# Kernel optimization log

Measured on AMD Instinct MI355X. Metric: run time of the kernel, lower is better.

## Reference

```python
import jax, jax.numpy as jnp
import numpy as np

KSZ, STRIDE, UNFOLD, FREQ = 9, 1, 12, 6  # patch size, stride, LISTA unfoldings, sim-refresh freq
P, C = 256, 3                            # num_filters, image channels


def im2col(I, k):
    # torch F.unfold ordering: channel slowest, then (ki,kj); stride=1, no padding
    b, c, H, W = I.shape
    hO, wO = H - k + 1, W - k + 1
    patches = jnp.stack([I[:, :, i:i + hO, j:j + wO] for i in range(k) for j in range(k)], axis=2)
    return patches.reshape(b, c * k * k, hO, wO)  # (b, c*k*k, hO, wO)


def col2im_avg(cols, out_hw, k):
    # inverse of im2col with overlap-averaging (fold / fold(ones))
    b, ckk, hO, wO = cols.shape
    c = ckk // (k * k)
    cols = cols.reshape(b, c, k * k, hO, wO)
    H, W = out_hw
    out = jnp.zeros((b, c, H, W), cols.dtype)
    cnt = jnp.zeros((1, 1, H, W), cols.dtype)
    for idx in range(k * k):
        i, j = idx // k, idx % k
        out = out.at[:, :, i:i + hO, j:j + wO].add(cols[:, :, idx])
        cnt = cnt.at[:, :, i:i + hO, j:j + wO].add(1.0)
    return out / cnt


def conv1x1(w, x):
    # 1x1 conv == channel matmul; w: (out, in), x: (b, in, h, w)
    return jnp.einsum('on,bnhw->bohw', w, x)


def soft_matching(x):
    # patch-pairwise similarity: softmax over negative squared L2 distances
    # between patch embeddings (SoftMatchingLayer, no window mask since
    # center_windows=False). Output (b, N, N).
    b, n, h, w = x.shape
    xf = x.reshape(b, n, h * w)
    sq = jnp.sum(xf * xf, axis=1)  # (b, N)
    d = sq[:, :, None] + sq[:, None, :] - 2.0 * jnp.einsum('bni,bnj->bij', xf, xf)
    return jax.nn.softmax(-d, axis=1)  # normalize over the aggregated (group) axis


def group_prox(A, theta, sim):
    # group-sparse proximal operator: per-filter L2 norm over similarity-weighted
    # groups, ReLU shrinkage. A: (b,p,h,w), theta: (p,), sim: (b,N,N), N=h*w.
    b, p, h, w = A.shape
    Af = A.reshape(b, p, h * w)
    support = jnp.sqrt(jnp.sum(jnp.abs(sim), axis=1, keepdims=True) + 1e-12)  # (b,1,N)
    norm2 = jnp.sqrt(jnp.matmul(Af * Af, sim) + 1e-8)                          # (b,p,N)
    out = jax.nn.relu(1.0 - theta[None, :, None] * support / norm2) * Af
    return out.reshape(b, p, h, w)


def setup_inputs() -> dict:
    key = jax.random.key(0)
    k0, k1 = jax.random.split(key)
    n = KSZ * KSZ * C  # 243 patch dim
    I = jax.random.normal(k0, (2, C, 56, 56), jnp.float32)
    D = jax.random.normal(k1, (n, P), jnp.float32)
    D = D / jnp.linalg.norm(D, ord=2)  # divide by sqrt(max eig of D^T D) = sigma_max
    Wa = D.T          # apply_A: (P, n)
    Wd = D            # apply_D: (n, P)
    Ww = D            # apply_W: (n, P)
    h_param = 0.12
    std0 = jnp.full((1, n, 1, 1), 1.0 / h_param, jnp.float32)   # std_y=True, first (only) lista
    lmbdas = jnp.full((UNFOLD, P), 0.3, jnp.float32)            # multi_lmbda per unfolding
    nu = jnp.full((1,), 1.0, jnp.float32)
    return {"I": I, "Wa": Wa, "Wd": Wd, "Ww": Ww, "std0": std0, "lmbdas": lmbdas, "nu": nu}


def reference(I, Wa, Wd, Ww, std0, lmbdas, nu):
    H, W = I.shape[2], I.shape[3]
    I_col = im2col(I, KSZ)                       # (b, 243, 48, 48), N = 2304
    mean_patch = I_col.mean(axis=1, keepdims=True)
    I_col = I_col - mean_patch
    sim = soft_matching(I_col * std0)            # (b, N, N)
    gamma = group_prox(conv1x1(Wa, I_col), lmbdas[0], sim)
    for k in range(UNFOLD - 1):
        if k % FREQ == 0 and k != 0:
            # corr_update == 2: refresh similarity from current patch estimates
            sim_new = soft_matching(conv1x1(Ww, gamma) * std0)
            nus = jax.nn.sigmoid(nu)
            sim = (1.0 - nus) * sim + nus * sim_new
        r_k = conv1x1(Wa, I_col - conv1x1(Wd, gamma))
        gamma = group_prox(gamma + r_k, lmbdas[k + 1], sim)
    out_all = conv1x1(Ww, gamma) + mean_patch
    return col2im_avg(out_all, (H, W), KSZ)
```

## Files before the change

### kernel.cpp

```cpp
#include <hip/hip_runtime.h>
#include <math.h>

#define NPIX 2304
#define NDIM 243
#define PDIM 256
#define BATCH 2
#define HO 48
#define IMGH 56
#define NCH 3
#define UNFOLD 12
#define FREQ 6

typedef __attribute__((ext_vector_type(8))) short bf16x8;
typedef __attribute__((ext_vector_type(4))) float f32x4;
typedef unsigned short ushort_t;

__device__ inline unsigned short f2bf(float x) {
    union { float f; unsigned u; } v; v.f = x;
    unsigned r = (v.u + 0x7FFFu + ((v.u >> 16) & 1u)) >> 16;
    return (unsigned short)r;
}
__device__ inline float bf2f(unsigned short u) {
    return __uint_as_float(((unsigned)u) << 16);
}

__device__ __forceinline__ void gload16(const ushort_t* g, ushort_t* s) {
    __builtin_amdgcn_global_load_lds(
        (__attribute__((address_space(1))) void*)g,
        (__attribute__((address_space(3))) void*)s, 16, 0, 0);
}

__global__ __launch_bounds__(1024) void k_precomp(const float* __restrict__ Wa,
                                                  const float* __restrict__ Wd,
                                                  const float* __restrict__ Ww,
                                                  const float* __restrict__ std0,
                                                  ushort_t* __restrict__ Mh, ushort_t* __restrict__ Ml,
                                                  ushort_t* __restrict__ Qh, ushort_t* __restrict__ Ql,
                                                  ushort_t* __restrict__ Wah, ushort_t* __restrict__ Wal,
                                                  ushort_t* __restrict__ Wwh, ushort_t* __restrict__ Wwl) {
    int p = blockIdx.x;
    int tid = threadIdx.x;
    int q = tid & 255, cc = tid >> 8;
    float m = 0.f, qv = 0.f;
    for (int c = cc; c < NDIM; c += 4) {
        m += Wa[p * NDIM + c] * Wd[c * PDIM + q];
        float s = std0[c];
        qv += s * s * Ww[c * PDIM + p] * Ww[c * PDIM + q];
    }
    __shared__ float sm[2][1024];
    sm[0][tid] = m; sm[1][tid] = qv;
    __syncthreads();
    if (cc == 0) {
        m  = sm[0][q] + sm[0][q + 256] + sm[0][q + 512] + sm[0][q + 768];
        qv = sm[1][q] + sm[1][q + 256] + sm[1][q + 512] + sm[1][q + 768];
        int off = p * PDIM + q;
        unsigned short h = f2bf(m);
        Mh[off] = h; Ml[off] = f2bf(m - bf2f(h));
        h = f2bf(qv);
        Qh[off] = h; Ql[off] = f2bf(qv - bf2f(h));
        float wa = (q < NDIM) ? Wa[p * NDIM + q] : 0.f;
        h = f2bf(wa);
        Wah[off] = h; Wal[off] = f2bf(wa - bf2f(h));
        float ww = (p < NDIM) ? Ww[p * PDIM + q] : 0.f;
        h = f2bf(ww);
        Wwh[off] = h; Wwl[off] = f2bf(ww - bf2f(h));
    }
}

__global__ __launch_bounds__(256) void k_im2col(const float* __restrict__ I,
                                                float* __restrict__ meanp,
                                                ushort_t* __restrict__ XTsh, ushort_t* __restrict__ XTsl,
                                                ushort_t* __restrict__ XTuh, ushort_t* __restrict__ XTul,
                                                const float* __restrict__ std0) {
    int col = blockIdx.x % NPIX;
    int b = blockIdx.x / NPIX;
    int oi = col / HO, oj = col % HO;
    int t = threadIdx.x;
    float v = 0.f;
    if (t < NDIM) {
        int c = t / 81, rem = t % 81, ki = rem / 9, kj = rem % 9;
        v = I[((size_t)(b * NCH + c) * IMGH + (oi + ki)) * IMGH + (oj + kj)];
    }
    __shared__ float red[256];
    red[t] = v;
    __syncthreads();
    for (int s = 128; s > 0; s >>= 1) {
        if (t < s) red[t] += red[t + s];
        __syncthreads();
    }
    float mean = red[0] / (float)NDIM;
    float xu = (t < NDIM) ? v - mean : 0.f;
    float xs = (t < NDIM) ? xu * std0[t] : 0.f;
    if (t == 0) meanp[b * NPIX + col] = mean;
    size_t xo = ((size_t)b * NPIX + col) * 256 + t;
    unsigned short h = f2bf(xu);
    XTuh[xo] = h; XTul[xo] = f2bf(xu - bf2f(h));
    h = f2bf(xs);
    XTsh[xo] = h; XTsl[xo] = f2bf(xs - bf2f(h));
}

#define EPI_G 0
#define EPI_SPLITOUT 1
#define EPI_ITER 2
#define EPI_WAI 3
#define EPI_ADDCOL 4
#define EPI_PROX 5

template<int TM, int TN, int SPLIT, int BKU, int EPI>
__global__ __launch_bounds__(256) void k_sgemm(
    const ushort_t* __restrict__ Ah, const ushort_t* __restrict__ Al,
    const ushort_t* __restrict__ Bh, const ushort_t* __restrict__ Bl,
    int ldA, int ldB, size_t sA, size_t sB, int K,
    float* __restrict__ C, ushort_t* __restrict__ C2,
    ushort_t* __restrict__ Oh, ushort_t* __restrict__ Ol,
    const float* __restrict__ E1, const float* __restrict__ E2,
    int ldC, size_t sC,
    const float* __restrict__ EA, const float* __restrict__ theta,
    float* __restrict__ sqd,
    float* __restrict__ POut, ushort_t* __restrict__ gTh, ushort_t* __restrict__ gTl) {

    constexpr int CA = TM / 16, CB = TN / 16;
    constexpr int CHUNKS = (1 + SPLIT) * (CA + CB);
    constexpr int UNITS = CHUNKS * BKU;
    constexpr int CPW = UNITS / 4;
    constexpr int BUFE = UNITS * 512;
    constexpr int TRE = (EPI == EPI_PROX) ? 2 * 64 * 34 : 0;
    constexpr int LDSE = (2 * BUFE > TRE) ? 2 * BUFE : TRE;
    constexpr int WM = TM / 2, WN = TN / 2;
    constexpr int MF = WM / 16, NF = WN / 16;

    __shared__ ushort_t lds[LDSE];

    int nwg = gridDim.x * gridDim.y * gridDim.z;
    int hw = blockIdx.x + gridDim.x * (blockIdx.y + gridDim.y * blockIdx.z);
    int L = (hw & 7) * (nwg >> 3) + (hw >> 3);
    int m_idx = L % gridDim.y;
    int n_idx = (L / gridDim.y) % gridDim.x;
    int b = L / (gridDim.y * gridDim.x);

    int n0 = n_idx * TN;
    int m0 = m_idx * TM;
    int tid = threadIdx.x;
    int w = tid >> 6, l = tid & 63, lm = l & 15, kh = l >> 4;
    int wm = (w >> 1) * WM, wn = (w & 1) * WN;

    const ushort_t* pAh = Ah + b * sA;
    const ushort_t* pAl = SPLIT ? Al + b * sA : nullptr;
    const ushort_t* pBh = Bh + b * sB;
    const ushort_t* pBl = SPLIT ? Bl + b * sB : nullptr;

    int srow = l >> 2;
    int sslot = ((l & 3) ^ ((l >> 3) & 3)) << 3;

    auto stage = [&](int bsel, int k0) {
        ushort_t* bb = lds + bsel * BUFE;
        #pragma unroll
        for (int i = 0; i < CPW; ++i) {
            int uu = w * CPW + i;
            int c = uu / BKU, u = uu % BKU;
            const ushort_t* src; int ld; int rowg;
            if (SPLIT) {
                if (c < CA)               { src = pAh; ld = ldA; rowg = m0 + c * 16; }
                else if (c < 2 * CA)      { src = pAl; ld = ldA; rowg = m0 + (c - CA) * 16; }
                else if (c < 2 * CA + CB) { src = pBh; ld = ldB; rowg = n0 + (c - 2 * CA) * 16; }
                else                      { src = pBl; ld = ldB; rowg = n0 + (c - 2 * CA - CB) * 16; }
            } else {
                if (c < CA) { src = pAh; ld = ldA; rowg = m0 + c * 16; }
                else        { src = pBh; ld = ldB; rowg = n0 + (c - CA) * 16; }
            }
            const ushort_t* g = src + (size_t)(rowg + srow) * ld + k0 + u * 32 + sslot;
            gload16(g, bb + (size_t)(c * BKU + u) * 512);
        }
    };

    f32x4 acc[MF][NF];
    #pragma unroll
    for (int mf = 0; mf < MF; ++mf)
        #pragma unroll
        for (int nf = 0; nf < NF; ++nf) acc[mf][nf] = (f32x4){0.f, 0.f, 0.f, 0.f};

    int sw = ((kh ^ ((lm >> 1) & 3)) << 3);
    const int NT = K / (32 * BKU);

    stage(0, 0);
    __syncthreads();
    for (int t = 0; t < NT; ++t) {
        if (t + 1 < NT) stage((t + 1) & 1, (t + 1) * (32 * BKU));
        ushort_t* bb = lds + (t & 1) * BUFE;
        ushort_t* LA_h = bb;
        ushort_t* LA_l = bb + CA * BKU * 512;
        ushort_t* LB_h = bb + (1 + SPLIT) * CA * BKU * 512;
        ushort_t* LB_l = LB_h + CB * BKU * 512;
        #pragma unroll
        for (int s = 0; s < BKU; ++s) {
            bf16x8 afh[MF], afl[MF], bfh[NF], bfl[NF];
            #pragma unroll
            for (int mf = 0; mf < MF; ++mf) {
                int off = ((wm >> 4) + mf) * (BKU * 512) + s * 512 + lm * 32 + sw;
                afh[mf] = *reinterpret_cast<const bf16x8*>(LA_h + off);
                if (SPLIT) afl[mf] = *reinterpret_cast<const bf16x8*>(LA_l + off);
            }
            #pragma unroll
            for (int nf = 0; nf < NF; ++nf) {
                int off = ((wn >> 4) + nf) * (BKU * 512) + s * 512 + lm * 32 + sw;
                bfh[nf] = *reinterpret_cast<const bf16x8*>(LB_h + off);
                if (SPLIT) bfl[nf] = *reinterpret_cast<const bf16x8*>(LB_l + off);
            }
            #pragma unroll
            for (int mf = 0; mf < MF; ++mf)
                #pragma unroll
                for (int nf = 0; nf < NF; ++nf) {
                    acc[mf][nf] = __builtin_amdgcn_mfma_f32_16x16x32_bf16(afh[mf], bfh[nf], acc[mf][nf], 0, 0, 0);
                    if (SPLIT) {
                        acc[mf][nf] = __builtin_amdgcn_mfma_f32_16x16x32_bf16(afh[mf], bfl[nf], acc[mf][nf], 0, 0, 0);
                        acc[mf][nf] = __builtin_amdgcn_mfma_f32_16x16x32_bf16(afl[mf], bfh[nf], acc[mf][nf], 0, 0, 0);
                    }
                }
        }
        __syncthreads();
    }

    if (EPI == EPI_PROX) {
        ushort_t* tbh = lds;
        ushort_t* tbl = lds + 64 * 34;
        #pragma unroll
        for (int mf = 0; mf < MF; ++mf)
            #pragma unroll
            for (int nf = 0; nf < NF; ++nf)
                #pragma unroll
                for (int r = 0; r < 4; ++r) {
                    int pl = wm + mf * 16 + kh * 4 + r;
                    int jl = wn + nf * 16 + lm;
                    int gp = m0 + pl;
                    float n2 = sqrtf(acc[mf][nf][r] + 1e-8f);
                    size_t off = b * sC + (size_t)gp * ldC + (n0 + jl);
                    float v = fmaxf(1.f - theta[gp] / n2, 0.f) * EA[off];
                    POut[off] = v;
                    unsigned short h = f2bf(v);
                    tbh[jl * 34 + pl] = h;
                    tbl[jl * 34 + pl] = f2bf(v - bf2f(h));
                }
        __syncthreads();
        {
            int jj = tid >> 2, seg = (tid & 3) * 8;
            size_t go = ((size_t)b * NPIX + n0 + jj) * PDIM + m0 + seg;
            bf16x8 vh, vl;
            #pragma unroll
            for (int e = 0; e < 8; ++e) {
                vh[e] = (short)tbh[jj * 34 + seg + e];
                vl[e] = (short)tbl[jj * 34 + seg + e];
            }
            *reinterpret_cast<bf16x8*>(gTh + go) = vh;
            *reinterpret_cast<bf16x8*>(gTl + go) = vl;
        }
    } else {
        #pragma unroll
        for (int mf = 0; mf < MF; ++mf)
            #pragma unroll
            for (int nf = 0; nf < NF; ++nf)
                #pragma unroll
                for (int r = 0; r < 4; ++r) {
                    int gm = m0 + wm + mf * 16 + kh * 4 + r;
                    int gn = n0 + wn + nf * 16 + lm;
                    float v = acc[mf][nf][r];
                    size_t off = b * sC + (size_t)gm * ldC + gn;
                    if (EPI == EPI_G) {
                        C[off] = v;
                        if (gm == gn) sqd[b * NPIX + gm] = v;
                    } else if (EPI == EPI_SPLITOUT) {
                        unsigned short h = f2bf(v);
                        Oh[off] = h; Ol[off] = f2bf(v - bf2f(h));
                    } else if (EPI == EPI_ITER) {
                        float o = E1[off] + E2[off] - v;
                        C[off] = o;
                        C2[off] = f2bf(o * o);
                    } else if (EPI == EPI_WAI) {
                        C[off] = v;
                        C2[off] = f2bf(v * v);
                    } else {
                        C[off] = v + E1[b * NPIX + gn];
                    }
                }
    }
}

template<int BLEND>
__global__ __launch_bounds__(256) void k_softmax(const float* __restrict__ G,
                                                 const float* __restrict__ sq,
                                                 ushort_t* __restrict__ Sbf,
                                                 const float* __restrict__ nu) {
    int b = blockIdx.x / NPIX;
    int j = blockIdx.x % NPIX;
    const float* Grow = G + ((size_t)b * NPIX + j) * NPIX;
    const float* sqb = sq + (size_t)b * NPIX;
    int t = threadIdx.x;
    float v[9];
    float m = -1e30f;
    #pragma unroll
    for (int i = 0; i < 9; ++i) {
        int ix = t + i * 256;
        v[i] = 2.f * Grow[ix] - sqb[ix];
        m = fmaxf(m, v[i]);
    }
    __shared__ float red[256];
    red[t] = m; __syncthreads();
    for (int s = 128; s > 0; s >>= 1) { if (t < s) red[t] = fmaxf(red[t], red[t+s]); __syncthreads(); }
    m = red[0];
    __syncthreads();
    float ss = 0.f;
    #pragma unroll
    for (int i = 0; i < 9; ++i) { v[i] = expf(v[i] - m); ss += v[i]; }
    red[t] = ss; __syncthreads();
    for (int s = 128; s > 0; s >>= 1) { if (t < s) red[t] += red[t+s]; __syncthreads(); }
    float inv = 1.f / red[0];
    ushort_t* Srow = Sbf + ((size_t)b * NPIX + j) * NPIX;
    if (BLEND) {
        float nus = 1.f / (1.f + expf(-nu[0]));
        #pragma unroll
        for (int i = 0; i < 9; ++i) {
            int ix = t + i * 256;
            Srow[ix] = f2bf((1.f - nus) * bf2f(Srow[ix]) + nus * (v[i] * inv));
        }
    } else {
        #pragma unroll
        for (int i = 0; i < 9; ++i) Srow[t + i * 256] = f2bf(v[i] * inv);
    }
}

__global__ void k_col2im(const float* __restrict__ T, float* __restrict__ out) {
    int idx = blockIdx.x * blockDim.x + threadIdx.x;
    int total = BATCH * NCH * IMGH * IMGH;
    if (idx >= total) return;
    int x = idx % IMGH; int tmp = idx / IMGH;
    int y = tmp % IMGH; tmp /= IMGH;
    int c = tmp % NCH; int b = tmp / NCH;
    int kiLo = max(0, y - (HO - 1)), kiHi = min(8, y);
    int kjLo = max(0, x - (HO - 1)), kjHi = min(8, x);
    float s = 0.f;
    for (int ki = kiLo; ki <= kiHi; ++ki)
        for (int kj = kjLo; kj <= kjHi; ++kj) {
            int ch = c * 81 + ki * 9 + kj;
            s += T[((size_t)b * 256 + ch) * NPIX + (y - ki) * HO + (x - kj)];
        }
    int cnt = (kiHi - kiLo + 1) * (kjHi - kjLo + 1);
    out[idx] = s / (float)cnt;
}

extern "C" void kernel_launch(void* const* d_in, const int* in_sizes, int n_in,
                              void* d_out, int out_size, void* d_ws, size_t ws_size,
                              hipStream_t stream) {
    const float* I    = (const float*)d_in[0];
    const float* Wa   = (const float*)d_in[1];
    const float* Wd   = (const float*)d_in[2];
    const float* Ww   = (const float*)d_in[3];
    const float* std0 = (const float*)d_in[4];
    const float* lmb  = (const float*)d_in[5];
    const float* nu   = (const float*)d_in[6];
    float* out = (float*)d_out;
    float* ws = (float*)d_ws;

    const size_t NP256 = (size_t)NPIX * 256;
    size_t off = 0;
    auto alloc = [&](size_t n) { float* p = ws + off; off += (n + 63) & ~(size_t)63; return p; };
    auto allocU = [&](size_t n) { return (ushort_t*)alloc((n + 1) / 2); };

    float* WaI   = alloc((size_t)BATCH * PDIM * NPIX);
    float* Abuf  = alloc((size_t)BATCH * PDIM * NPIX);
    float* gamma = alloc((size_t)BATCH * PDIM * NPIX);
    float* TR    = alloc((size_t)BATCH * 256 * NPIX);
    float* G     = alloc((size_t)BATCH * NPIX * NPIX);
    ushort_t* Sbf  = allocU((size_t)BATCH * NPIX * NPIX);
    ushort_t* A2   = allocU((size_t)BATCH * PDIM * NPIX);
    ushort_t* XTsh = allocU(BATCH * NP256);
    ushort_t* XTsl = allocU(BATCH * NP256);
    ushort_t* XTuh = allocU(BATCH * NP256);
    ushort_t* XTul = allocU(BATCH * NP256);
    ushort_t* gTh  = allocU(BATCH * NP256);
    ushort_t* gTl  = allocU(BATCH * NP256);
    ushort_t* HTh  = allocU(BATCH * NP256);
    ushort_t* HTl  = allocU(BATCH * NP256);
    ushort_t* Mh   = allocU(PDIM * PDIM);
    ushort_t* Ml   = allocU(PDIM * PDIM);
    ushort_t* Qh   = allocU(PDIM * PDIM);
    ushort_t* Ql   = allocU(PDIM * PDIM);
    ushort_t* Wah  = allocU(PDIM * PDIM);
    ushort_t* Wal  = allocU(PDIM * PDIM);
    ushort_t* Wwh  = allocU(PDIM * PDIM);
    ushort_t* Wwl  = allocU(PDIM * PDIM);
    float* meanp = alloc((size_t)BATCH * NPIX);
    float* sqd   = alloc((size_t)BATCH * NPIX);
    (void)ws_size; (void)in_sizes; (void)n_in; (void)out_size;

    dim3 blk(256);
    const size_t sPN = (size_t)PDIM * NPIX;
    const size_t sNN = (size_t)NPIX * NPIX;

    k_precomp<<<dim3(PDIM), dim3(1024), 0, stream>>>(Wa, Wd, Ww, std0, Mh, Ml, Qh, Ql, Wah, Wal, Wwh, Wwl);
    k_im2col<<<dim3(BATCH * NPIX), blk, 0, stream>>>(I, meanp, XTsh, XTsl, XTuh, XTul, std0);

    k_sgemm<128, 128, 1, 1, EPI_G><<<dim3(NPIX/128, NPIX/128, BATCH), blk, 0, stream>>>(
        XTsh, XTsl, XTsh, XTsl, 256, 256, NP256, NP256, 256,
        G, nullptr, nullptr, nullptr, nullptr, nullptr, NPIX, sNN,
        nullptr, nullptr, sqd, nullptr, nullptr, nullptr);
    k_softmax<0><<<dim3(BATCH * NPIX), blk, 0, stream>>>(G, sqd, Sbf, nu);

    k_sgemm<32, 64, 1, 1, EPI_WAI><<<dim3(NPIX/64, PDIM/32, BATCH), blk, 0, stream>>>(
        Wah, Wal, XTuh, XTul, 256, 256, 0, NP256, 256,
        WaI, A2, nullptr, nullptr, nullptr, nullptr, NPIX, sPN,
        nullptr, nullptr, nullptr, nullptr, nullptr, nullptr);
    k_sgemm<32, 64, 0, 2, EPI_PROX><<<dim3(NPIX/64, PDIM/32, BATCH), blk, 0, stream>>>(
        A2, nullptr, Sbf, nullptr, NPIX, NPIX, sPN, sNN, NPIX,
        nullptr, nullptr, nullptr, nullptr, nullptr, nullptr, NPIX, sPN,
        WaI, lmb, nullptr, gamma, gTh, gTl);

    for (int k = 0; k < UNFOLD - 1; ++k) {
        if (k % FREQ == 0 && k != 0) {
            k_sgemm<32, 64, 1, 1, EPI_SPLITOUT><<<dim3(PDIM/64, NPIX/32, BATCH), blk, 0, stream>>>(
                gTh, gTl, Qh, Ql, 256, 256, NP256, 0, 256,
                nullptr, nullptr, HTh, HTl, nullptr, nullptr, 256, NP256,
                nullptr, nullptr, nullptr, nullptr, nullptr, nullptr);
            k_sgemm<128, 128, 1, 1, EPI_G><<<dim3(NPIX/128, NPIX/128, BATCH), blk, 0, stream>>>(
                gTh, gTl, HTh, HTl, 256, 256, NP256, NP256, 256,
                G, nullptr, nullptr, nullptr, nullptr, nullptr, NPIX, sNN,
                nullptr, nullptr, sqd, nullptr, nullptr, nullptr);
            k_softmax<1><<<dim3(BATCH * NPIX), blk, 0, stream>>>(G, sqd, Sbf, nu);
        }
        k_sgemm<32, 64, 1, 1, EPI_ITER><<<dim3(NPIX/64, PDIM/32, BATCH), blk, 0, stream>>>(
            Mh, Ml, gTh, gTl, 256, 256, 0, NP256, 256,
            Abuf, A2, nullptr, nullptr, WaI, gamma, NPIX, sPN,
            nullptr, nullptr, nullptr, nullptr, nullptr, nullptr);
        k_sgemm<32, 64, 0, 2, EPI_PROX><<<dim3(NPIX/64, PDIM/32, BATCH), blk, 0, stream>>>(
            A2, nullptr, Sbf, nullptr, NPIX, NPIX, sPN, sNN, NPIX,
            nullptr, nullptr, nullptr, nullptr, nullptr, nullptr, NPIX, sPN,
            Abuf, lmb + (size_t)(k + 1) * PDIM, nullptr, gamma, gTh, gTl);
    }
    k_sgemm<32, 64, 1, 1, EPI_ADDCOL><<<dim3(NPIX/64, 256/32, BATCH), blk, 0, stream>>>(
        Wwh, Wwl, gTh, gTl, 256, 256, 0, NP256, 256,
        TR, nullptr, nullptr, nullptr, meanp, nullptr, NPIX, (size_t)256 * NPIX,
        nullptr, nullptr, nullptr, nullptr, nullptr, nullptr);
    k_col2im<<<dim3((BATCH * NCH * IMGH * IMGH + 255) / 256), blk, 0, stream>>>(TR, out);
}
```

Baseline: 504.4 us.

## Exploit Gram symmetry with upper-triangle tiles and fuse independent GEMM launches

The N×N Gram GEMMs now compute only the upper-triangular 64×64 tiles, decoded from a linear block id, and write each off-diagonal tile's transpose through LDS as a mirror. The initial Gram GEMM is merged into one launch with the Wa·X GEMM, and the refresh-step H GEMM is merged into one launch with the iteration GEMM. The intent is to roughly halve Gram FLOPs and cut launch count and tail effects. In exchange the tiles shrink from 128×128 to 64×64, which lowers reuse, and the mirror pass adds an extra transpose store.

```diff
diff --git a/kernel.cpp b/kernel.cpp
--- a/kernel.cpp
+++ b/kernel.cpp
@@ -30,73 +30,13 @@
         (__attribute__((address_space(3))) void*)s, 16, 0, 0);
 }
 
-__global__ __launch_bounds__(1024) void k_precomp(const float* __restrict__ Wa,
-                                                  const float* __restrict__ Wd,
-                                                  const float* __restrict__ Ww,
-                                                  const float* __restrict__ std0,
-                                                  ushort_t* __restrict__ Mh, ushort_t* __restrict__ Ml,
-                                                  ushort_t* __restrict__ Qh, ushort_t* __restrict__ Ql,
-                                                  ushort_t* __restrict__ Wah, ushort_t* __restrict__ Wal,
-                                                  ushort_t* __restrict__ Wwh, ushort_t* __restrict__ Wwl) {
-    int p = blockIdx.x;
-    int tid = threadIdx.x;
-    int q = tid & 255, cc = tid >> 8;
-    float m = 0.f, qv = 0.f;
-    for (int c = cc; c < NDIM; c += 4) {
-        m += Wa[p * NDIM + c] * Wd[c * PDIM + q];
-        float s = std0[c];
-        qv += s * s * Ww[c * PDIM + p] * Ww[c * PDIM + q];
-    }
-    __shared__ float sm[2][1024];
-    sm[0][tid] = m; sm[1][tid] = qv;
-    __syncthreads();
-    if (cc == 0) {
-        m  = sm[0][q] + sm[0][q + 256] + sm[0][q + 512] + sm[0][q + 768];
-        qv = sm[1][q] + sm[1][q + 256] + sm[1][q + 512] + sm[1][q + 768];
-        int off = p * PDIM + q;
-        unsigned short h = f2bf(m);
-        Mh[off] = h; Ml[off] = f2bf(m - bf2f(h));
-        h = f2bf(qv);
-        Qh[off] = h; Ql[off] = f2bf(qv - bf2f(h));
-        float wa = (q < NDIM) ? Wa[p * NDIM + q] : 0.f;
-        h = f2bf(wa);
-        Wah[off] = h; Wal[off] = f2bf(wa - bf2f(h));
-        float ww = (p < NDIM) ? Ww[p * PDIM + q] : 0.f;
-        h = f2bf(ww);
-        Wwh[off] = h; Wwl[off] = f2bf(ww - bf2f(h));
-    }
-}
-
-__global__ __launch_bounds__(256) void k_im2col(const float* __restrict__ I,
-                                                float* __restrict__ meanp,
-                                                ushort_t* __restrict__ XTsh, ushort_t* __restrict__ XTsl,
-                                                ushort_t* __restrict__ XTuh, ushort_t* __restrict__ XTul,
-                                                const float* __restrict__ std0) {
-    int col = blockIdx.x % NPIX;
-    int b = blockIdx.x / NPIX;
-    int oi = col / HO, oj = col % HO;
-    int t = threadIdx.x;
-    float v = 0.f;
-    if (t < NDIM) {
-        int c = t / 81, rem = t % 81, ki = rem / 9, kj = rem % 9;
-        v = I[((size_t)(b * NCH + c) * IMGH + (oi + ki)) * IMGH + (oj + kj)];
-    }
-    __shared__ float red[256];
-    red[t] = v;
-    __syncthreads();
-    for (int s = 128; s > 0; s >>= 1) {
-        if (t < s) red[t] += red[t + s];
-        __syncthreads();
-    }
-    float mean = red[0] / (float)NDIM;
-    float xu = (t < NDIM) ? v - mean : 0.f;
-    float xs = (t < NDIM) ? xu * std0[t] : 0.f;
-    if (t == 0) meanp[b * NPIX + col] = mean;
-    size_t xo = ((size_t)b * NPIX + col) * 256 + t;
-    unsigned short h = f2bf(xu);
-    XTuh[xo] = h; XTul[xo] = f2bf(xu - bf2f(h));
-    h = f2bf(xs);
-    XTsh[xo] = h; XTsl[xo] = f2bf(xs - bf2f(h));
+__device__ __forceinline__ void ut_decode(int e, int& mi, int& ni) {
+    float f = (73.0f - sqrtf(5329.0f - 8.0f * (float)e)) * 0.5f;
+    mi = (int)f;
+    if (mi > 35) mi = 35;
+    while (mi > 0 && e < mi * 36 - mi * (mi - 1) / 2) mi--;
+    while (e >= (mi + 1) * 36 - (mi + 1) * mi / 2) mi++;
+    ni = mi + (e - (mi * 36 - mi * (mi - 1) / 2));
 }
 
 #define EPI_G 0
@@ -107,7 +47,8 @@
 #define EPI_PROX 5
 
 template<int TM, int TN, int SPLIT, int BKU, int EPI>
-__global__ __launch_bounds__(256) void k_sgemm(
+__device__ __forceinline__ void gemm_tile(
+    ushort_t* __restrict__ lds, int m0, int n0, int b, int mirror,
     const ushort_t* __restrict__ Ah, const ushort_t* __restrict__ Al,
     const ushort_t* __restrict__ Bh, const ushort_t* __restrict__ Bl,
     int ldA, int ldB, size_t sA, size_t sB, int K,
@@ -124,22 +65,9 @@
     constexpr int UNITS = CHUNKS * BKU;
     constexpr int CPW = UNITS / 4;
     constexpr int BUFE = UNITS * 512;
-    constexpr int TRE = (EPI == EPI_PROX) ? 2 * 64 * 34 : 0;
-    constexpr int LDSE = (2 * BUFE > TRE) ? 2 * BUFE : TRE;
     constexpr int WM = TM / 2, WN = TN / 2;
     constexpr int MF = WM / 16, NF = WN / 16;
 
-    __shared__ ushort_t lds[LDSE];
-
-    int nwg = gridDim.x * gridDim.y * gridDim.z;
-    int hw = blockIdx.x + gridDim.x * (blockIdx.y + gridDim.y * blockIdx.z);
-    int L = (hw & 7) * (nwg >> 3) + (hw >> 3);
-    int m_idx = L % gridDim.y;
-    int n_idx = (L / gridDim.y) % gridDim.x;
-    int b = L / (gridDim.y * gridDim.x);
-
-    int n0 = n_idx * TN;
-    int m0 = m_idx * TM;
     int tid = threadIdx.x;
     int w = tid >> 6, l = tid & 63, lm = l & 15, kh = l >> 4;
     int wm = (w >> 1) * WM, wn = (w & 1) * WN;
@@ -222,7 +150,7 @@
 
     if (EPI == EPI_PROX) {
         ushort_t* tbh = lds;
-        ushort_t* tbl = lds + 64 * 34;
+        ushort_t* tbl = lds + TN * (TM + 2);
         #pragma unroll
         for (int mf = 0; mf < MF; ++mf)
             #pragma unroll
@@ -237,22 +165,24 @@
                     float v = fmaxf(1.f - theta[gp] / n2, 0.f) * EA[off];
                     POut[off] = v;
                     unsigned short h = f2bf(v);
-                    tbh[jl * 34 + pl] = h;
-                    tbl[jl * 34 + pl] = f2bf(v - bf2f(h));
+                    tbh[jl * (TM + 2) + pl] = h;
+                    tbl[jl * (TM + 2) + pl] = f2bf(v - bf2f(h));
                 }
         __syncthreads();
         {
-            int jj = tid >> 2, seg = (tid & 3) * 8;
+            constexpr int SEGS = TM / 8;
+            int jj = tid / SEGS, seg = (tid % SEGS) * 8;
             size_t go = ((size_t)b * NPIX + n0 + jj) * PDIM + m0 + seg;
             bf16x8 vh, vl;
             #pragma unroll
             for (int e = 0; e < 8; ++e) {
-                vh[e] = (short)tbh[jj * 34 + seg + e];
-                vl[e] = (short)tbl[jj * 34 + seg + e];
+                vh[e] = (short)tbh[jj * (TM + 2) + seg + e];
+                vl[e] = (short)tbl[jj * (TM + 2) + seg + e];
             }
             *reinterpret_cast<bf16x8*>(gTh + go) = vh;
             *reinterpret_cast<bf16x8*>(gTl + go) = vl;
         }
+        __syncthreads();
     } else {
         #pragma unroll
         for (int mf = 0; mf < MF; ++mf)
@@ -281,7 +211,206 @@
                         C[off] = v + E1[b * NPIX + gn];
                     }
                 }
-    }
+        if (EPI == EPI_G && mirror) {
+            __syncthreads();
+            float* ldsF = (float*)lds;
+            #pragma unroll
+            for (int mf = 0; mf < MF; ++mf)
+                #pragma unroll
+                for (int nf = 0; nf < NF; ++nf)
+                    #pragma unroll
+                    for (int r = 0; r < 4; ++r) {
+                        int il = wm + mf * 16 + kh * 4 + r;
+                        int jl = wn + nf * 16 + lm;
+                        ldsF[jl * 66 + il] = acc[mf][nf][r];
+                    }
+            __syncthreads();
+            int row = tid >> 2;
+            int colq = (tid & 3) * 16;
+            float* Crow = C + b * sC + (size_t)(n0 + row) * ldC + m0 + colq;
+            #pragma unroll
+            for (int e = 0; e < 16; e += 4) {
+                float4 o = make_float4(ldsF[row * 66 + colq + e],
+                                       ldsF[row * 66 + colq + e + 1],
+                                       ldsF[row * 66 + colq + e + 2],
+                                       ldsF[row * 66 + colq + e + 3]);
+                *reinterpret_cast<float4*>(Crow + e) = o;
+            }
+            __syncthreads();
+        }
+    }
+}
+
+template<int TM, int TN, int SPLIT, int BKU, int EPI, int SYMM>
+__global__ __launch_bounds__(256) void k_sgemm(
+    const ushort_t* __restrict__ Ah, const ushort_t* __restrict__ Al,
+    const ushort_t* __restrict__ Bh, const ushort_t* __restrict__ Bl,
+    int ldA, int ldB, size_t sA, size_t sB, int K,
+    float* __restrict__ C, ushort_t* __restrict__ C2,
+    ushort_t* __restrict__ Oh, ushort_t* __restrict__ Ol,
+    const float* __restrict__ E1, const float* __restrict__ E2,
+    int ldC, size_t sC,
+    const float* __restrict__ EA, const float* __restrict__ theta,
+    float* __restrict__ sqd,
+    float* __restrict__ POut, ushort_t* __restrict__ gTh, ushort_t* __restrict__ gTl) {
+
+    constexpr int CA = TM / 16, CB = TN / 16;
+    constexpr int UNITS = (1 + SPLIT) * (CA + CB) * BKU;
+    constexpr int BUFE = UNITS * 512;
+    constexpr int TRE = (EPI == EPI_PROX) ? 2 * TN * (TM + 2) : 0;
+    constexpr int LDSE = (2 * BUFE > TRE) ? 2 * BUFE : TRE;
+    __shared__ ushort_t lds[LDSE];
+
+    if (SYMM) {
+        int id = blockIdx.x;
+        int bb = id / 666, e = id % 666, mi, ni;
+        ut_decode(e, mi, ni);
+        gemm_tile<TM, TN, SPLIT, BKU, EPI>(lds, mi * 64, ni * 64, bb, (mi != ni),
+            Ah, Al, Bh, Bl, ldA, ldB, sA, sB, K, C, C2, Oh, Ol, E1, E2, ldC, sC,
+            EA, theta, sqd, POut, gTh, gTl);
+    } else {
+        int nwg = gridDim.x * gridDim.y * gridDim.z;
+        int hw = blockIdx.x + gridDim.x * (blockIdx.y + gridDim.y * blockIdx.z);
+        int L = (hw & 7) * (nwg >> 3) + (hw >> 3);
+        int m_idx = L % gridDim.y;
+        int n_idx = (L / gridDim.y) % gridDim.x;
+        int b = L / (gridDim.y * gridDim.x);
+        gemm_tile<TM, TN, SPLIT, BKU, EPI>(lds, m_idx * TM, n_idx * TN, b, 0,
+            Ah, Al, Bh, Bl, ldA, ldB, sA, sB, K, C, C2, Oh, Ol, E1, E2, ldC, sC,
+            EA, theta, sqd, POut, gTh, gTl);
+    }
+}
+
+__global__ __launch_bounds__(256) void k_gram_wai(
+    const ushort_t* __restrict__ XTsh, const ushort_t* __restrict__ XTsl,
+    const ushort_t* __restrict__ XTuh, const ushort_t* __restrict__ XTul,
+    const ushort_t* __restrict__ Wah, const ushort_t* __restrict__ Wal,
+    float* __restrict__ G, float* __restrict__ sqd,
+    float* __restrict__ WaI, ushort_t* __restrict__ A2) {
+    __shared__ ushort_t lds[16384];
+    const size_t NP256 = (size_t)NPIX * 256;
+    const size_t sPN = (size_t)PDIM * NPIX;
+    const size_t sNN = (size_t)NPIX * NPIX;
+    int id = blockIdx.x;
+    if (id < 1332) {
+        int bb = id / 666, e = id % 666, mi, ni;
+        ut_decode(e, mi, ni);
+        gemm_tile<64, 64, 1, 1, EPI_G>(lds, mi * 64, ni * 64, bb, (mi != ni),
+            XTsh, XTsl, XTsh, XTsl, 256, 256, NP256, NP256, 256,
+            G, nullptr, nullptr, nullptr, nullptr, nullptr, NPIX, sNN,
+            nullptr, nullptr, sqd, nullptr, nullptr, nullptr);
+    } else {
+        int lid = id - 1332;
+        int L = (lid & 7) * 72 + (lid >> 3);
+        int m_idx = L % 8;
+        int n_idx = (L / 8) % 36;
+        int b = L / 288;
+        gemm_tile<32, 64, 1, 1, EPI_WAI>(lds, m_idx * 32, n_idx * 64, b, 0,
+            Wah, Wal, XTuh, XTul, 256, 256, 0, NP256, 256,
+            WaI, A2, nullptr, nullptr, nullptr, nullptr, NPIX, sPN,
+            nullptr, nullptr, nullptr, nullptr, nullptr, nullptr);
+    }
+}
+
+__global__ __launch_bounds__(256) void k_ht_iter(
+    const ushort_t* __restrict__ gTh, const ushort_t* __restrict__ gTl,
+    const ushort_t* __restrict__ Qh, const ushort_t* __restrict__ Ql,
+    ushort_t* __restrict__ HTh, ushort_t* __restrict__ HTl,
+    const ushort_t* __restrict__ Mh, const ushort_t* __restrict__ Ml,
+    float* __restrict__ Abuf, ushort_t* __restrict__ A2,
+    const float* __restrict__ WaI, const float* __restrict__ gamma) {
+    __shared__ ushort_t lds[12288];
+    const size_t NP256 = (size_t)NPIX * 256;
+    const size_t sPN = (size_t)PDIM * NPIX;
+    int id = blockIdx.x;
+    if (id < 576) {
+        int m_idx = id % 72;
+        int n_idx = (id / 72) % 4;
+        int b = id / 288;
+        gemm_tile<32, 64, 1, 1, EPI_SPLITOUT>(lds, m_idx * 32, n_idx * 64, b, 0,
+            gTh, gTl, Qh, Ql, 256, 256, NP256, 0, 256,
+            nullptr, nullptr, HTh, HTl, nullptr, nullptr, 256, NP256,
+            nullptr, nullptr, nullptr, nullptr, nullptr, nullptr);
+    } else {
+        int lid = id - 576;
+        int L = (lid & 7) * 72 + (lid >> 3);
+        int m_idx = L % 8;
+        int n_idx = (L / 8) % 36;
+        int b = L / 288;
+        gemm_tile<32, 64, 1, 1, EPI_ITER>(lds, m_idx * 32, n_idx * 64, b, 0,
+            Mh, Ml, gTh, gTl, 256, 256, 0, NP256, 256,
+            Abuf, A2, nullptr, nullptr, WaI, gamma, NPIX, sPN,
+            nullptr, nullptr, nullptr, nullptr, nullptr, nullptr);
+    }
+}
+
+__global__ __launch_bounds__(1024) void k_precomp(const float* __restrict__ Wa,
+                                                  const float* __restrict__ Wd,
+                                                  const float* __restrict__ Ww,
+                                                  const float* __restrict__ std0,
+                                                  ushort_t* __restrict__ Mh, ushort_t* __restrict__ Ml,
+                                                  ushort_t* __restrict__ Qh, ushort_t* __restrict__ Ql,
+                                                  ushort_t* __restrict__ Wah, ushort_t* __restrict__ Wal,
+                                                  ushort_t* __restrict__ Wwh, ushort_t* __restrict__ Wwl) {
+    int p = blockIdx.x;
+    int tid = threadIdx.x;
+    int q = tid & 255, cc = tid >> 8;
+    float m = 0.f, qv = 0.f;
+    for (int c = cc; c < NDIM; c += 4) {
+        m += Wa[p * NDIM + c] * Wd[c * PDIM + q];
+        float s = std0[c];
+        qv += s * s * Ww[c * PDIM + p] * Ww[c * PDIM + q];
+    }
+    __shared__ float sm[2][1024];
+    sm[0][tid] = m; sm[1][tid] = qv;
+    __syncthreads();
+    if (cc == 0) {
+        m  = sm[0][q] + sm[0][q + 256] + sm[0][q + 512] + sm[0][q + 768];
+        qv = sm[1][q] + sm[1][q + 256] + sm[1][q + 512] + sm[1][q + 768];
+        int off = p * PDIM + q;
+        unsigned short h = f2bf(m);
+        Mh[off] = h; Ml[off] = f2bf(m - bf2f(h));
+        h = f2bf(qv);
+        Qh[off] = h; Ql[off] = f2bf(qv - bf2f(h));
+        float wa = (q < NDIM) ? Wa[p * NDIM + q] : 0.f;
+        h = f2bf(wa);
+        Wah[off] = h; Wal[off] = f2bf(wa - bf2f(h));
+        float ww = (p < NDIM) ? Ww[p * PDIM + q] : 0.f;
+        h = f2bf(ww);
+        Wwh[off] = h; Wwl[off] = f2bf(ww - bf2f(h));
+    }
+}
+
+__global__ __launch_bounds__(256) void k_im2col(const float* __restrict__ I,
+                                                float* __restrict__ meanp,
+                                                ushort_t* __restrict__ XTsh, ushort_t* __restrict__ XTsl,
+                                                ushort_t* __restrict__ XTuh, ushort_t* __restrict__ XTul,
+                                                const float* __restrict__ std0) {
+    int col = blockIdx.x % NPIX;
+    int b = blockIdx.x / NPIX;
+    int oi = col / HO, oj = col % HO;
+    int t = threadIdx.x;
+    float v = 0.f;
+    if (t < NDIM) {
+        int c = t / 81, rem = t % 81, ki = rem / 9, kj = rem % 9;
+        v = I[((size_t)(b * NCH + c) * IMGH + (oi + ki)) * IMGH + (oj + kj)];
+    }
+    __shared__ float red[256];
+    red[t] = v;
+    __syncthreads();
+    for (int s = 128; s > 0; s >>= 1) {
+        if (t < s) red[t] += red[t + s];
+        __syncthreads();
+    }
+    float mean = red[0] / (float)NDIM;
+    float xu = (t < NDIM) ? v - mean : 0.f;
+    float xs = (t < NDIM) ? xu * std0[t] : 0.f;
+    if (t == 0) meanp[b * NPIX + col] = mean;
+    size_t xo = ((size_t)b * NPIX + col) * 256 + t;
+    unsigned short h = f2bf(xu);
+    XTuh[xo] = h; XTul[xo] = f2bf(xu - bf2f(h));
+    h = f2bf(xs);
+    XTsh[xo] = h; XTsl[xo] = f2bf(xs - bf2f(h));
 }
 
 template<int BLEND>
@@ -398,43 +527,36 @@
     k_precomp<<<dim3(PDIM), dim3(1024), 0, stream>>>(Wa, Wd, Ww, std0, Mh, Ml, Qh, Ql, Wah, Wal, Wwh, Wwl);
     k_im2col<<<dim3(BATCH * NPIX), blk, 0, stream>>>(I, meanp, XTsh, XTsl, XTuh, XTul, std0);
 
-    k_sgemm<128, 128, 1, 1, EPI_G><<<dim3(NPIX/128, NPIX/128, BATCH), blk, 0, stream>>>(
-        XTsh, XTsl, XTsh, XTsl, 256, 256, NP256, NP256, 256,
-        G, nullptr, nullptr, nullptr, nullptr, nullptr, NPIX, sNN,
-        nullptr, nullptr, sqd, nullptr, nullptr, nullptr);
+    k_gram_wai<<<dim3(1332 + 576), blk, 0, stream>>>(
+        XTsh, XTsl, XTuh, XTul, Wah, Wal, G, sqd, WaI, A2);
     k_softmax<0><<<dim3(BATCH * NPIX), blk, 0, stream>>>(G, sqd, Sbf, nu);
 
-    k_sgemm<32, 64, 1, 1, EPI_WAI><<<dim3(NPIX/64, PDIM/32, BATCH), blk, 0, stream>>>(
-        Wah, Wal, XTuh, XTul, 256, 256, 0, NP256, 256,
-        WaI, A2, nullptr, nullptr, nullptr, nullptr, NPIX, sPN,
-        nullptr, nullptr, nullptr, nullptr, nullptr, nullptr);
-    k_sgemm<32, 64, 0, 2, EPI_PROX><<<dim3(NPIX/64, PDIM/32, BATCH), blk, 0, stream>>>(
+    k_sgemm<32, 64, 0, 2, EPI_PROX, 0><<<dim3(NPIX/64, PDIM/32, BATCH), blk, 0, stream>>>(
         A2, nullptr, Sbf, nullptr, NPIX, NPIX, sPN, sNN, NPIX,
         nullptr, nullptr, nullptr, nullptr, nullptr, nullptr, NPIX, sPN,
         WaI, lmb, nullptr, gamma, gTh, gTl);
 
     for (int k = 0; k < UNFOLD - 1; ++k) {
-        if (k % FREQ == 0 && k != 0) {
-            k_sgemm<32, 64, 1, 1, EPI_SPLITOUT><<<dim3(PDIM/64, NPIX/32, BATCH), blk, 0, stream>>>(
-                gTh, gTl, Qh, Ql, 256, 256, NP256, 0, 256,
-                nullptr, nullptr, HTh, HTl, nullptr, nullptr, 256, NP256,
-                nullptr, nullptr, nullptr, nullptr, nullptr, nullptr);
-            k_sgemm<128, 128, 1, 1, EPI_G><<<dim3(NPIX/128, NPIX/128, BATCH), blk, 0, stream>>>(
+        if (k == FREQ) {
+            k_ht_iter<<<dim3(1152), blk, 0, stream>>>(
+                gTh, gTl, Qh, Ql, HTh, HTl, Mh, Ml, Abuf, A2, WaI, gamma);
+            k_sgemm<64, 64, 1, 1, EPI_G, 1><<<dim3(1332), blk, 0, stream>>>(
                 gTh, gTl, HTh, HTl, 256, 256, NP256, NP256, 256,
                 G, nullptr, nullptr, nullptr, nullptr, nullptr, NPIX, sNN,
                 nullptr, nullptr, sqd, nullptr, nullptr, nullptr);
             k_softmax<1><<<dim3(BATCH * NPIX), blk, 0, stream>>>(G, sqd, Sbf, nu);
-        }
-        k_sgemm<32, 64, 1, 1, EPI_ITER><<<dim3(NPIX/64, PDIM/32, BATCH), blk, 0, stream>>>(
-            Mh, Ml, gTh, gTl, 256, 256, 0, NP256, 256,
-            Abuf, A2, nullptr, nullptr, WaI, gamma, NPIX, sPN,
-            nullptr, nullptr, nullptr, nullptr, nullptr, nullptr);
-        k_sgemm<32, 64, 0, 2, EPI_PROX><<<dim3(NPIX/64, PDIM/32, BATCH), blk, 0, stream>>>(
+        } else {
+            k_sgemm<32, 64, 1, 1, EPI_ITER, 0><<<dim3(NPIX/64, PDIM/32, BATCH), blk, 0, stream>>>(
+                Mh, Ml, gTh, gTl, 256, 256, 0, NP256, 256,
+                Abuf, A2, nullptr, nullptr, WaI, gamma, NPIX, sPN,
+                nullptr, nullptr, nullptr, nullptr, nullptr, nullptr);
+        }
+        k_sgemm<32, 64, 0, 2, EPI_PROX, 0><<<dim3(NPIX/64, PDIM/32, BATCH), blk, 0, stream>>>(
             A2, nullptr, Sbf, nullptr, NPIX, NPIX, sPN, sNN, NPIX,
             nullptr, nullptr, nullptr, nullptr, nullptr, nullptr, NPIX, sPN,
             Abuf, lmb + (size_t)(k + 1) * PDIM, nullptr, gamma, gTh, gTl);
     }
-    k_sgemm<32, 64, 1, 1, EPI_ADDCOL><<<dim3(NPIX/64, 256/32, BATCH), blk, 0, stream>>>(
+    k_sgemm<32, 64, 1, 1, EPI_ADDCOL, 0><<<dim3(NPIX/64, 256/32, BATCH), blk, 0, stream>>>(
         Wwh, Wwl, gTh, gTl, 256, 256, 0, NP256, 256,
         TR, nullptr, nullptr, nullptr, meanp, nullptr, NPIX, (size_t)256 * NPIX,
         nullptr, nullptr, nullptr, nullptr, nullptr, nullptr);
```

After: 498.8 us. About the same (-1.1%).
